# Performance work log

Hardware: AMD Instinct MI355X
Metric: run time of the kernel (lower is better)

Reference implementation:

```python
import jax, jax.numpy as jnp
import numpy as np


def setup_inputs() -> dict:
    key = jax.random.key(0)
    ks = jax.random.split(key, 5)
    B, S, E, H, D = 4, 2048, 1024, 16, 64
    sc = 1.0 / np.sqrt(E)
    x = jax.random.normal(ks[0], (B, S, E), dtype=jnp.float32)
    Wq = jax.random.normal(ks[1], (H, E, D), dtype=jnp.float32) * sc
    Wk = jax.random.normal(ks[2], (H, E, D), dtype=jnp.float32) * sc
    Wv = jax.random.normal(ks[3], (H, E, D), dtype=jnp.float32) * sc
    Wo = jax.random.normal(ks[4], (E, E), dtype=jnp.float32) * sc
    bo = jnp.zeros((E,), dtype=jnp.float32)
    return {"x": x, "Wq": Wq, "Wk": Wk, "Wv": Wv, "Wo": Wo, "bo": bo}


def reference(x, Wq, Wk, Wv, Wo, bo):
    # x: [B,S,E]; Wq/Wk/Wv: [H,E,D]; Wo: [E,E]; bo: [E]
    B, S, E = x.shape
    H, _, D = Wq.shape
    q = jnp.einsum('bse,hed->bhsd', x, Wq)
    k = jnp.einsum('bse,hed->bhsd', x, Wk)
    v = jnp.einsum('bse,hed->bhsd', x, Wv)
    scale = jnp.asarray(D, x.dtype) ** -0.5
    att = jnp.einsum('bhsd,bhtd->bhst', q, k) * scale  # [B,H,S,S]
    causal = jnp.tril(jnp.ones((S, S), dtype=bool))
    att = jnp.where(causal, att, jnp.asarray(-jnp.inf, att.dtype))
    att = jax.nn.softmax(att, axis=-1)
    out = jnp.einsum('bhst,bhtd->bhsd', att, v)  # [B,H,S,D]
    # concat heads in order (head dim-major on last axis), then project
    out = out.transpose(0, 2, 1, 3).reshape(B, S, H * D)
    return out @ Wo.T + bo
```

## Files before the change

### kernel.cpp

```cpp
#include <hip/hip_runtime.h>
#include <hip/hip_bf16.h>

#define BB 4
#define SS 2048
#define EE 1024
#define HH 16
#define DD 64
#define MM (BB*SS)
#define HD (HH*DD)
#define NQKV (3*HD)

typedef __bf16 bf16_t;
typedef __bf16 bf16x4 __attribute__((ext_vector_type(4)));
typedef __bf16 bf16x8 __attribute__((ext_vector_type(8)));
typedef float f32x4 __attribute__((ext_vector_type(4)));

#define MFMA16(a,b,c) __builtin_amdgcn_mfma_f32_16x16x32_bf16(a,b,c,0,0,0)
#define NEG_INF (-__builtin_huge_valf())
#define QSCALE 0.1803368801111204f
#define CSHIFT 12.0f

__device__ __forceinline__ void gload_lds16(const void* g, void* l) {
  __builtin_amdgcn_global_load_lds((const __attribute__((address_space(1))) unsigned int*)g,
                                   (__attribute__((address_space(3))) unsigned int*)l,
                                   16, 0, 0);
}

#define SBAR() __builtin_amdgcn_s_barrier()
#define SCHB() __builtin_amdgcn_sched_barrier(0)
#define VMCNT6 do { asm volatile("s_waitcnt vmcnt(6)" ::: "memory"); } while(0)
#define VMCNT2 do { asm volatile("s_waitcnt vmcnt(2)" ::: "memory"); } while(0)
#define VMCNT0 do { asm volatile("s_waitcnt vmcnt(0)" ::: "memory"); } while(0)

__global__ __launch_bounds__(256)
void k_f32_to_bf16(const float* __restrict__ in, bf16_t* __restrict__ out, int n8) {
  int i = blockIdx.x*256 + threadIdx.x;
  if (i >= n8) return;
  const float4* p = reinterpret_cast<const float4*>(in) + (size_t)i*2;
  float4 a = p[0], b = p[1];
  bf16x8 o;
  o[0]=(bf16_t)a.x; o[1]=(bf16_t)a.y; o[2]=(bf16_t)a.z; o[3]=(bf16_t)a.w;
  o[4]=(bf16_t)b.x; o[5]=(bf16_t)b.y; o[6]=(bf16_t)b.z; o[7]=(bf16_t)b.w;
  *reinterpret_cast<bf16x8*>(out + (size_t)i*8) = o;
}

__global__ __launch_bounds__(256)
void k_conv_wqkv(const float* __restrict__ Wq, const float* __restrict__ Wk,
                 const float* __restrict__ Wv, bf16_t* __restrict__ Wt) {
  __shared__ float t[64][65];
  int wh = blockIdx.x;
  int which = wh >> 4, h = wh & 15;
  int e0 = blockIdx.y * 64;
  const float* W = (which==0) ? Wq : (which==1) ? Wk : Wv;
  const float* src = W + (size_t)h*EE*DD;
  int r = threadIdx.x >> 6, c = threadIdx.x & 63;
  #pragma unroll
  for (int i = 0; i < 16; ++i) {
    int e = i*4 + r;
    t[e][c] = src[(size_t)(e0+e)*DD + c];
  }
  __syncthreads();
  bf16_t* dst = Wt + (size_t)(which*HD + h*DD)*EE;
  #pragma unroll
  for (int i = 0; i < 16; ++i) {
    int d = i*4 + r;
    dst[(size_t)d*EE + e0 + c] = (bf16_t)t[c][d];
  }
}

#define NKT 16
template<int EPI, int NTX>
__global__ __launch_bounds__(512, 1)
void k_gemm8(const bf16_t* __restrict__ Ag, const bf16_t* __restrict__ Bg0,
             bf16_t* __restrict__ Qp, bf16_t* __restrict__ Kp, bf16_t* __restrict__ Vtp,
             const float* __restrict__ bias, float* __restrict__ Cout) {
  __shared__ __align__(16) bf16_t Ab[3][128*64];
  __shared__ __align__(16) bf16_t Bb[3][256*64];

  int orig = blockIdx.x;
  int xcd = orig & 7, lidx = orig >> 3;
  int tileY = xcd*8 + (lidx & 7);
  int tileX = lidx >> 3;
  int n0 = tileX * 256, m0 = tileY * 128;

  int tid = threadIdx.x;
  int lane = tid & 63, w = tid >> 6;
  int wr = w >> 2, wc = w & 3;
  int lr = lane & 15, lg = lane >> 4;

  const bf16_t* Bg = Bg0 + (size_t)n0 * EE;

  int r3 = tid >> 3;
  int gch = (tid & 7) ^ (r3 & 7);
  int ldsb = w * 1024;

#define STAGE_A(buf, kt) do { \
    const bf16_t* g_ = Ag + (size_t)(m0 + r3)*EE + (kt)*64 + gch*8; \
    char* l_ = (char*)Ab[buf] + ldsb; \
    gload_lds16(g_, l_); \
    gload_lds16(g_ + (size_t)64*EE, l_ + 8192); \
  } while(0)
#define STAGE_B(buf, kt, half) do { \
    const bf16_t* g_ = Bg + (size_t)((half)*128 + r3)*EE + (kt)*64 + gch*8; \
    char* l_ = (char*)Bb[buf] + (half)*16384 + ldsb; \
    gload_lds16(g_, l_); \
    gload_lds16(g_ + (size_t)64*EE, l_ + 8192); \
  } while(0)

  int sA = lr & 7;
  unsigned aoff[2] = { (unsigned)((wr*64 + lr)*128 + ((lg     ^ sA) << 4)),
                       (unsigned)((wr*64 + lr)*128 + (((4+lg) ^ sA) << 4)) };
  unsigned boff[2] = { (unsigned)((wc*64 + lr)*128 + ((lg     ^ sA) << 4)),
                       (unsigned)((wc*64 + lr)*128 + (((4+lg) ^ sA) << 4)) };

  f32x4 acc[4][4];
  #pragma unroll
  for (int i=0;i<4;i++)
    #pragma unroll
    for (int j=0;j<4;j++) acc[i][j] = (f32x4){0.f,0.f,0.f,0.f};
  bf16x8 af[2][4], bq[2][4];

#define PHASE1(buf, STAGE_STMT, WAITV) do { \
    _Pragma("unroll") for (int kh_=0; kh_<2; ++kh_) { \
      _Pragma("unroll") for (int mf_=0; mf_<4; ++mf_) \
        af[kh_][mf_] = *reinterpret_cast<const bf16x8*>((const char*)Ab[buf] + aoff[kh_] + mf_*2048); \
      _Pragma("unroll") for (int nf_=0; nf_<4; ++nf_) \
        bq[kh_][nf_] = *reinterpret_cast<const bf16x8*>((const char*)Bb[buf] + boff[kh_] + nf_*2048); \
    } \
    STAGE_STMT; \
    SBAR(); \
    asm volatile("s_waitcnt lgkmcnt(0)" ::: "memory"); \
    SCHB(); \
    __builtin_amdgcn_s_setprio(1); \
    _Pragma("unroll") for (int kh_=0; kh_<2; ++kh_) \
      _Pragma("unroll") for (int mf_=0; mf_<4; ++mf_) \
        _Pragma("unroll") for (int nf_=0; nf_<4; ++nf_) \
          acc[mf_][nf_] = MFMA16(af[kh_][mf_], bq[kh_][nf_], acc[mf_][nf_]); \
    __builtin_amdgcn_s_setprio(0); \
    WAITV; \
    SBAR(); \
    SCHB(); \
  } while(0)

  STAGE_A(0, 0); STAGE_B(0, 0, 0); STAGE_B(0, 0, 1);
  STAGE_A(1, 1); STAGE_B(1, 1, 0); STAGE_B(1, 1, 1);
  VMCNT6;
  SBAR();
  SCHB();

  #pragma unroll
  for (int t = 0; t < NKT; ++t) {
    int cur = t % 3, pre = (t+2) % 3;
    bool more = (t+2 < NKT);
    PHASE1(cur,
           if (more) { STAGE_A(pre, t+2); STAGE_B(pre, t+2, 0); STAGE_B(pre, t+2, 1); },
           { if (more) { VMCNT6; } else { VMCNT0; } });
  }
#undef PHASE1
#undef STAGE_A
#undef STAGE_B

  if (EPI == 0) {
    int which = n0 >> 10;
    if (which < 2) {
      #pragma unroll
      for (int mf=0; mf<4; ++mf) {
        #pragma unroll
        for (int nf=0; nf<4; ++nf) {
          int n = n0 + wc*64 + nf*16 + lr;
          int hd = n & 1023, h2 = hd >> 6, d = hd & 63;
          #pragma unroll
          for (int r=0;r<4;r++) {
            int m = m0 + wr*64 + mf*16 + lg*4 + r;
            int b = m >> 11, s = m & 2047;
            size_t bh = (size_t)(b*HH + h2);
            if (which == 0) Qp[(bh*SS + s)*DD + d] = (bf16_t)(acc[mf][nf][r] * QSCALE);
            else            Kp[(bh*SS + s)*DD + d] = (bf16_t)acc[mf][nf][r];
          }
        }
      }
    } else {
      #pragma unroll
      for (int mf=0; mf<4; ++mf) {
        #pragma unroll
        for (int nf=0; nf<4; ++nf) {
          int n = n0 + wc*64 + nf*16 + lr;
          int hd = n & 1023, h2 = hd >> 6, d = hd & 63;
          int m = m0 + wr*64 + mf*16 + lg*4;
          int b = m >> 11, s = m & 2047;
          size_t bh = (size_t)(b*HH + h2);
          bf16x4 vv;
          vv[0] = (bf16_t)acc[mf][nf][0];
          vv[1] = (bf16_t)acc[mf][nf][1];
          vv[2] = (bf16_t)acc[mf][nf][2];
          vv[3] = (bf16_t)acc[mf][nf][3];
          *reinterpret_cast<bf16x4*>(Vtp + (bh*DD + d)*SS + s) = vv;
        }
      }
    }
  } else {
    float bv[4];
    #pragma unroll
    for (int nf=0;nf<4;nf++) bv[nf] = bias[n0 + wc*64 + nf*16 + lr];
    #pragma unroll
    for (int mf=0; mf<4; ++mf)
      #pragma unroll
      for (int nf=0; nf<4; ++nf) {
        int n = n0 + wc*64 + nf*16 + lr;
        #pragma unroll
        for (int r=0;r<4;r++) {
          int m = m0 + wr*64 + mf*16 + lg*4 + r;
          Cout[(size_t)m*HD + n] = acc[mf][nf][r] + bv[nf];
        }
      }
  }
}

__global__ __launch_bounds__(512)
void k_attn(const bf16_t* __restrict__ Q, const bf16_t* __restrict__ K,
            const bf16_t* __restrict__ Vt, bf16_t* __restrict__ AO) {
  __shared__ __align__(16) bf16_t Ks[3][64*64];
  __shared__ __align__(16) bf16_t Vs[3][64*64];

  int id = blockIdx.x;
  int m8 = id & 7, d8 = id >> 3;
  int bh = m8*8 + (d8 >> 3);
  int u  = d8 & 7;

  int tid = threadIdx.x, lane = tid & 63, w = tid >> 6;
  int lr = lane & 15, lg = lane >> 4;
  const bf16_t* Qb = Q  + (size_t)bh * SS * DD;
  const bf16_t* Kp = K  + (size_t)bh * SS * DD;
  const bf16_t* Vp = Vt + (size_t)bh * DD * SS;
  int b = bh >> 4, h = bh & 15;

  int srow = tid >> 3;
  int gchunk = (tid & 7) ^ (srow & 7);

  bf16x8 onesf;
  #pragma unroll
  for (int i=0;i<8;i++) onesf[i] = (bf16_t)1.0f;

#define STAGE_KV(t, buf) do { \
    int kv0_ = (t)*64; \
    gload_lds16(Kp + (size_t)(kv0_ + srow)*DD + gchunk*8, (char*)Ks[buf] + w*1024); \
    gload_lds16(Vp + (size_t)srow*SS + kv0_ + gchunk*8,   (char*)Vs[buf] + w*1024); \
  } while(0)

  for (int ph = 0; ph < 2; ++ph) {
    int p = ph ? (15 - u) : u;
    int nt = 2*p + 2;
    int qrow0 = p*128 + w*16;
    int q = qrow0 + lr;

    bf16x8 qf[2];
    #pragma unroll
    for (int kk=0;kk<2;kk++)
      qf[kk] = *reinterpret_cast<const bf16x8*>(Qb + (size_t)(qrow0 + lr)*DD + kk*32 + lg*8);

    f32x4 po[4];
    #pragma unroll
    for (int i=0;i<4;i++) po[i] = (f32x4){0.f,0.f,0.f,0.f};
    f32x4 acclv = (f32x4){0.f,0.f,0.f,0.f};

    STAGE_KV(0, 0);
    STAGE_KV(1, 1);
    for (int t = 0; t < nt; ++t) {
      if (t < nt-1) { VMCNT2; } else { VMCNT0; }
      SBAR();
      SCHB();
      if (t+2 < nt) STAGE_KV(t+2, (t+2)%3);
      int kv0 = t*64;
      if (kv0 > qrow0 + 15) continue;
      int buf = t % 3;
      const bf16_t* Kb = Ks[buf];
      const bf16_t* Vb = Vs[buf];

      f32x4 sa[4];
      #pragma unroll
      for (int ct=0; ct<4; ++ct) {
        int rr = ct*16 + lr;
        int sw = rr & 7;
        bf16x8 k0 = *reinterpret_cast<const bf16x8*>(Kb + rr*64 + ((lg     ^ sw) << 3));
        bf16x8 k1 = *reinterpret_cast<const bf16x8*>(Kb + rr*64 + (((4+lg) ^ sw) << 3));
        f32x4 c = (f32x4){0.f,0.f,0.f,0.f};
        c = MFMA16(k0, qf[0], c);
        c = MFMA16(k1, qf[1], c);
        sa[ct] = c;
      }
      if (kv0 + 63 > qrow0) {
        #pragma unroll
        for (int ct=0;ct<4;ct++) {
          #pragma unroll
          for (int r=0;r<4;r++) {
            int kv = kv0 + ct*16 + lg*4 + r;
            if (kv > q) sa[ct][r] = NEG_INF;
          }
        }
      }
      bf16x8 pf[2];
      #pragma unroll
      for (int ct=0;ct<4;ct++)
        #pragma unroll
        for (int r=0;r<4;r++)
          pf[ct>>1][(ct&1)*4 + r] = (bf16_t)__builtin_amdgcn_exp2f(sa[ct][r] - CSHIFT);
      acclv = MFMA16(onesf, pf[0], acclv);
      acclv = MFMA16(onesf, pf[1], acclv);
      #pragma unroll
      for (int ctd=0; ctd<4; ++ctd) {
        int rr = ctd*16 + lr;
        int sw8 = rr & 7;
        int sub = (lg & 1) << 3;
        const char* rowb = (const char*)Vb + rr*128;
        #pragma unroll
        for (int kk=0; kk<2; ++kk) {
          int c0 = kk*4 + (lg>>1);
          bf16x4 lo = *reinterpret_cast<const bf16x4*>(rowb + (((c0     ^ sw8) << 4) | sub));
          bf16x4 hi = *reinterpret_cast<const bf16x4*>(rowb + ((((c0+2) ^ sw8) << 4) | sub));
          bf16x8 vf;
          vf[0]=lo[0]; vf[1]=lo[1]; vf[2]=lo[2]; vf[3]=lo[3];
          vf[4]=hi[0]; vf[5]=hi[1]; vf[6]=hi[2]; vf[7]=hi[3];
          po[ctd] = MFMA16(vf, pf[kk], po[ctd]);
        }
      }
    }
    SBAR();
    {
      float inv = 1.0f / acclv[0];
      bf16_t* dst = AO + (size_t)(b*SS + q)*HD + h*DD;
      #pragma unroll
      for (int ctd=0;ctd<4;ctd++) {
        bf16x4 vv;
        #pragma unroll
        for (int r=0;r<4;r++) vv[r] = (bf16_t)(po[ctd][r] * inv);
        *reinterpret_cast<bf16x4*>(dst + ctd*16 + lg*4) = vv;
      }
    }
  }
#undef STAGE_KV
}

extern "C" void kernel_launch(void* const* d_in, const int* in_sizes, int n_in,
                              void* d_out, int out_size, void* d_ws, size_t ws_size,
                              hipStream_t stream) {
  const float* x  = (const float*)d_in[0];
  const float* Wq = (const float*)d_in[1];
  const float* Wk = (const float*)d_in[2];
  const float* Wv = (const float*)d_in[3];
  const float* Wo = (const float*)d_in[4];
  const float* bo = (const float*)d_in[5];
  float* out = (float*)d_out;

  char* ws = (char*)d_ws;
  bf16_t* xb  = (bf16_t*)(ws + 0);
  bf16_t* wt  = (bf16_t*)(ws + 16777216);
  bf16_t* wob = (bf16_t*)(ws + 23068672);
  bf16_t* Qb  = (bf16_t*)(ws + 25165824);
  bf16_t* Kb  = (bf16_t*)(ws + 41943040);
  bf16_t* Vtb = (bf16_t*)(ws + 58720256);
  bf16_t* AO  = (bf16_t*)(ws + 75497472);

  k_f32_to_bf16<<<(MM*EE/8)/256, 256, 0, stream>>>(x,  xb,  MM*EE/8);
  k_f32_to_bf16<<<(EE*EE/8)/256, 256, 0, stream>>>(Wo, wob, EE*EE/8);
  dim3 gw(48, 16);
  k_conv_wqkv<<<gw, 256, 0, stream>>>(Wq, Wk, Wv, wt);

  k_gemm8<0,12><<<768, 512, 0, stream>>>(xb, wt, Qb, Kb, Vtb, nullptr, nullptr);

  k_attn<<<BB*HH*8, 512, 0, stream>>>(Qb, Kb, Vtb, AO);

  k_gemm8<1,4><<<256, 512, 0, stream>>>(AO, wob, nullptr, nullptr, nullptr, bo, out);
}
```

Measured before the change: 162.2 us.

## Add BK=32 QKV GEMM kernel with smaller LDS footprint for higher occupancy

Adds a new QKV projection GEMM variant that stages 32-wide K tiles instead of 64, shrinking the triple-buffered LDS footprint, and declares launch bounds allowing multiple blocks per CU. The goal is to overlap more blocks per CU and so hide memory latency better in the QKV projection. The trade-off is twice as many pipeline iterations, each with two barriers and fewer MFMAs between them, which adds more sync overhead per unit of work. The output projection keeps the old kernel.

```diff
diff --git a/kernel.cpp b/kernel.cpp
--- a/kernel.cpp
+++ b/kernel.cpp
@@ -29,6 +29,7 @@
 #define SBAR() __builtin_amdgcn_s_barrier()
 #define SCHB() __builtin_amdgcn_sched_barrier(0)
 #define VMCNT6 do { asm volatile("s_waitcnt vmcnt(6)" ::: "memory"); } while(0)
+#define VMCNT3 do { asm volatile("s_waitcnt vmcnt(3)" ::: "memory"); } while(0)
 #define VMCNT2 do { asm volatile("s_waitcnt vmcnt(2)" ::: "memory"); } while(0)
 #define VMCNT0 do { asm volatile("s_waitcnt vmcnt(0)" ::: "memory"); } while(0)
 
@@ -65,6 +66,141 @@
   for (int i = 0; i < 16; ++i) {
     int d = i*4 + r;
     dst[(size_t)d*EE + e0 + c] = (bf16_t)t[c][d];
+  }
+}
+
+template<int EPI, int NTX>
+__global__ __launch_bounds__(512, 4)
+void k_gemm32(const bf16_t* __restrict__ Ag, const bf16_t* __restrict__ Bg0,
+              bf16_t* __restrict__ Qp, bf16_t* __restrict__ Kp, bf16_t* __restrict__ Vtp,
+              const float* __restrict__ bias, float* __restrict__ Cout) {
+  __shared__ __align__(16) bf16_t Ab[3][128*32];
+  __shared__ __align__(16) bf16_t Bb[3][256*32];
+
+  int orig = blockIdx.x;
+  int xcd = orig & 7, lidx = orig >> 3;
+  int tileY = xcd*8 + (lidx & 7);
+  int tileX = lidx >> 3;
+  int n0 = tileX * 256, m0 = tileY * 128;
+
+  int tid = threadIdx.x;
+  int lane = tid & 63, w = tid >> 6;
+  int wr = w >> 2, wc = w & 3;
+  int lr = lane & 15, lg = lane >> 4;
+
+  const bf16_t* Bg = Bg0 + (size_t)n0 * EE;
+
+  int r4 = tid >> 2;
+  int gch = (tid & 3) ^ ((tid >> 3) & 3);
+  int ldsb = w * 1024;
+
+#define STAGE_A32(buf, kt) \
+    gload_lds16(Ag + (size_t)(m0 + r4)*EE + (kt)*32 + gch*8, (char*)Ab[buf] + ldsb)
+#define STAGE_B32(buf, kt, half) \
+    gload_lds16(Bg + (size_t)((half)*128 + r4)*EE + (kt)*32 + gch*8, \
+                (char*)Bb[buf] + (half)*8192 + ldsb)
+
+  int swA = (lr >> 1) & 3;
+  unsigned aoff = (unsigned)((wr*64 + lr)*64 + ((lg ^ swA) << 4));
+  unsigned boff = (unsigned)((wc*64 + lr)*64 + ((lg ^ swA) << 4));
+
+  f32x4 acc[4][4];
+  #pragma unroll
+  for (int i=0;i<4;i++)
+    #pragma unroll
+    for (int j=0;j<4;j++) acc[i][j] = (f32x4){0.f,0.f,0.f,0.f};
+  bf16x8 af[4], bq[4];
+
+#define PHASE32(buf, STAGE_STMT, WAITV) do { \
+    _Pragma("unroll") for (int mf_=0; mf_<4; ++mf_) \
+      af[mf_] = *reinterpret_cast<const bf16x8*>((const char*)Ab[buf] + aoff + mf_*1024); \
+    _Pragma("unroll") for (int nf_=0; nf_<4; ++nf_) \
+      bq[nf_] = *reinterpret_cast<const bf16x8*>((const char*)Bb[buf] + boff + nf_*1024); \
+    STAGE_STMT; \
+    SBAR(); \
+    asm volatile("s_waitcnt lgkmcnt(0)" ::: "memory"); \
+    SCHB(); \
+    __builtin_amdgcn_s_setprio(1); \
+    _Pragma("unroll") for (int mf_=0; mf_<4; ++mf_) \
+      _Pragma("unroll") for (int nf_=0; nf_<4; ++nf_) \
+        acc[mf_][nf_] = MFMA16(af[mf_], bq[nf_], acc[mf_][nf_]); \
+    __builtin_amdgcn_s_setprio(0); \
+    WAITV; \
+    SBAR(); \
+    SCHB(); \
+  } while(0)
+
+  STAGE_A32(0, 0); STAGE_B32(0, 0, 0); STAGE_B32(0, 0, 1);
+  STAGE_A32(1, 1); STAGE_B32(1, 1, 0); STAGE_B32(1, 1, 1);
+  VMCNT3;
+  SBAR();
+  SCHB();
+
+  #pragma unroll
+  for (int t = 0; t < 32; ++t) {
+    int cur = t % 3, pre = (t+2) % 3;
+    bool more = (t+2 < 32);
+    PHASE32(cur,
+            if (more) { STAGE_A32(pre, t+2); STAGE_B32(pre, t+2, 0); STAGE_B32(pre, t+2, 1); },
+            { if (more) { VMCNT3; } else { VMCNT0; } });
+  }
+#undef PHASE32
+#undef STAGE_A32
+#undef STAGE_B32
+
+  if (EPI == 0) {
+    int which = n0 >> 10;
+    if (which < 2) {
+      #pragma unroll
+      for (int mf=0; mf<4; ++mf) {
+        #pragma unroll
+        for (int nf=0; nf<4; ++nf) {
+          int n = n0 + wc*64 + nf*16 + lr;
+          int hd = n & 1023, h2 = hd >> 6, d = hd & 63;
+          #pragma unroll
+          for (int r=0;r<4;r++) {
+            int m = m0 + wr*64 + mf*16 + lg*4 + r;
+            int b = m >> 11, s = m & 2047;
+            size_t bh = (size_t)(b*HH + h2);
+            if (which == 0) Qp[(bh*SS + s)*DD + d] = (bf16_t)(acc[mf][nf][r] * QSCALE);
+            else            Kp[(bh*SS + s)*DD + d] = (bf16_t)acc[mf][nf][r];
+          }
+        }
+      }
+    } else {
+      #pragma unroll
+      for (int mf=0; mf<4; ++mf) {
+        #pragma unroll
+        for (int nf=0; nf<4; ++nf) {
+          int n = n0 + wc*64 + nf*16 + lr;
+          int hd = n & 1023, h2 = hd >> 6, d = hd & 63;
+          int m = m0 + wr*64 + mf*16 + lg*4;
+          int b = m >> 11, s = m & 2047;
+          size_t bh = (size_t)(b*HH + h2);
+          bf16x4 vv;
+          vv[0] = (bf16_t)acc[mf][nf][0];
+          vv[1] = (bf16_t)acc[mf][nf][1];
+          vv[2] = (bf16_t)acc[mf][nf][2];
+          vv[3] = (bf16_t)acc[mf][nf][3];
+          *reinterpret_cast<bf16x4*>(Vtp + (bh*DD + d)*SS + s) = vv;
+        }
+      }
+    }
+  } else {
+    float bv[4];
+    #pragma unroll
+    for (int nf=0;nf<4;nf++) bv[nf] = bias[n0 + wc*64 + nf*16 + lr];
+    #pragma unroll
+    for (int mf=0; mf<4; ++mf)
+      #pragma unroll
+      for (int nf=0; nf<4; ++nf) {
+        int n = n0 + wc*64 + nf*16 + lr;
+        #pragma unroll
+        for (int r=0;r<4;r++) {
+          int m = m0 + wr*64 + mf*16 + lg*4 + r;
+          Cout[(size_t)m*HD + n] = acc[mf][nf][r] + bv[nf];
+        }
+      }
   }
 }
 
@@ -365,7 +501,7 @@
   dim3 gw(48, 16);
   k_conv_wqkv<<<gw, 256, 0, stream>>>(Wq, Wk, Wv, wt);
 
-  k_gemm8<0,12><<<768, 512, 0, stream>>>(xb, wt, Qb, Kb, Vtb, nullptr, nullptr);
+  k_gemm32<0,12><<<768, 512, 0, stream>>>(xb, wt, Qb, Kb, Vtb, nullptr, nullptr);
 
   k_attn<<<BB*HH*8, 512, 0, stream>>>(Qb, Kb, Vtb, AO);
 
```

Result: faster. 157.8 us (-2.7%).
